# Kernel optimization log

Hardware: AMD Instinct MI355X
Metric: run time of the kernel (lower is better)

The kernel has to match this reference:

```python
import jax, jax.numpy as jnp
import numpy as np

BETA1 = 0.9
BETA2 = 0.8
THRESH = 1.0  # snntorch Leaky default threshold

T, B, NI, NH, NO = 100, 1024, 256, 512, 10


def setup_inputs() -> dict:
    key = jax.random.key(0)
    kx, k1, k2 = jax.random.split(key, 3)
    x = jax.random.normal(kx, (T, B, NI), dtype=jnp.float32)
    # Weight_synapse 'bin_random_prob' init: binary {0, w} with given probs
    W1 = (jax.random.uniform(k1, (NH, NI)) < 0.8).astype(jnp.float32) * 0.5
    W2 = (jax.random.uniform(k2, (NO, NH)) < 0.5).astype(jnp.float32) * 0.5
    return {"x": x, "W1": W1, "W2": W2}


def _lif(mem, cur, beta):
    # snntorch Leaky, reset_mechanism='subtract': reset from previous mem,
    # then mem = beta*mem + cur - reset*threshold; spk = heaviside(mem - thr)
    reset = (mem > THRESH).astype(cur.dtype)
    mem = beta * mem + cur - reset * THRESH
    spk = (mem > THRESH).astype(cur.dtype)
    return spk, mem


def reference(x, W1, W2):
    b = x.shape[1]
    mem1_0 = jnp.zeros((b, W1.shape[0]), x.dtype)
    mem2_0 = jnp.zeros((b, W2.shape[0]), x.dtype)

    def step(carry, xt):
        mem1, mem2 = carry
        cur1 = xt @ W1.T                      # [B, NH]
        spk1, mem1 = _lif(mem1, cur1, BETA1)
        cur2 = spk1 @ W2.T                    # [B, NO]
        spk2, mem2 = _lif(mem2, cur2, BETA2)
        return (mem1, mem2), (cur1, cur2, spk1, spk2, mem1, mem2)

    _, (cur1, cur2, spk1, spk2, mem1, mem2) = jax.lax.scan(step, (mem1_0, mem2_0), x)
    # matches {'cur':[c1,c2],'spks':[s1,s2],'mem':[m1,m2]}, each stacked on time
    return cur1, cur2, spk1, spk2, mem1, mem2
```

## Files before the change

kernel.cpp:

```cpp
#include <hip/hip_runtime.h>

#define TT 100
#define BB 1024
#define NI 256
#define NH 512
#define NO 10
#define TB (TT*BB)
#define GK 512
#define GN 512

constexpr long long C1_OFF = 0;
constexpr long long C2_OFF = 52428800LL;
constexpr long long S1_OFF = 53452800LL;
constexpr long long S2_OFF = 105881600LL;
constexpr long long M1_OFF = 106905600LL;
constexpr long long M2_OFF = 159334400LL;

typedef short bf16x8 __attribute__((ext_vector_type(8)));
typedef float f32x4 __attribute__((ext_vector_type(4)));

__device__ __forceinline__ unsigned int rne_bf16(float f) {
    unsigned int u = __float_as_uint(f);
    return (u + 0x7fffu + ((u >> 16) & 1u)) >> 16;
}

__device__ __forceinline__ unsigned int pack_hilo(float f) {
    unsigned int hi = rne_bf16(f);
    float hif = __uint_as_float(hi << 16);
    float e = f - hif;
    unsigned int lo = rne_bf16(e);
    return (hi & 0xffffu) | (lo << 16);
}

__device__ __forceinline__ void pack4(uint4& d, const float4& a) {
    d.x = pack_hilo(a.x); d.y = pack_hilo(a.y); d.z = pack_hilo(a.z); d.w = pack_hilo(a.w);
}

__device__ __forceinline__ void gload16(const void* g, void* l) {
    __builtin_amdgcn_global_load_lds(
        (const __attribute__((address_space(1))) void*)g,
        (__attribute__((address_space(3))) void*)l, 16, 0, 0);
}

__global__ void prep_w_kernel(const float* __restrict__ W1, short* __restrict__ Wimg) {
    int i = blockIdx.x * blockDim.x + threadIdx.x;
    if (i >= 4 * 16 * 128 * 4) return;
    int c16 = i & 3;
    int r   = (i >> 2) & 127;
    int kt  = (i >> 9) & 15;
    int p   = i >> 13;
    int usrc = c16 ^ ((r >> 1) & 3);
    int kbase = kt * 16 + usrc * 4;
    float4 w = *(const float4*)&W1[(long long)(p * 128 + r) * NI + kbase];
    float f[4] = {w.x, w.y, w.z, w.w};
    uint4 o;
    unsigned int* op = &o.x;
    #pragma unroll
    for (int j = 0; j < 4; ++j) {
        unsigned int hb = __float_as_uint(f[j]) >> 16;
        op[j] = hb | (hb << 16);
    }
    ((uint4*)Wimg)[i] = o;
}

__launch_bounds__(256, 2)
__global__ void gemm1_kernel(const float* __restrict__ x, const short* __restrict__ Wimg,
                             float* __restrict__ C) {
    __shared__ short As[2][128][40];
    __shared__ short Ws[2][128][32];
    const int tid = threadIdx.x;
    const int bid = blockIdx.x;
    const int x8 = bid & 7;
    const int g  = bid >> 3;
    const int p  = g & 3;
    const int panel = (g >> 2) * 8 + x8;
    const int m0 = (799 - panel) * 128;
    const int n0 = p * 128;
    const int wid = tid >> 6;
    const int lane = tid & 63;
    const int wm = (wid >> 1) * 64;
    const int wn = (wid & 1) * 64;

    f32x4 acc[4][4] = {};

    const int srow = tid >> 2;
    const int sc4 = tid & 3;
    const long long ax0 = (long long)(m0 + srow) * NI + sc4 * 4;
    const long long ax1 = ax0 + 64LL * NI;

    const int fr = lane & 15;
    const int fk = (lane >> 4) * 8;
    const int swz = (((lane >> 4) ^ ((fr >> 1) & 3)) << 4);

    const short* wbase = Wimg + (long long)p * 16 * 4096;
    const int c0 = wid * 2;

    gload16(wbase + (c0    ) * 512 + lane * 8, (char*)&Ws[0][0][0] + (c0    ) * 1024);
    gload16(wbase + (c0 + 1) * 512 + lane * 8, (char*)&Ws[0][0][0] + (c0 + 1) * 1024);
    uint4 pa0, pa1;
    {
        float4 t0a = *(const float4*)&x[ax0];
        float4 t0b = *(const float4*)&x[ax1];
        uint4 q0, q1;
        pack4(q0, t0a); pack4(q1, t0b);
        *(uint4*)&As[0][srow][sc4 * 8]      = q0;
        *(uint4*)&As[0][srow + 64][sc4 * 8] = q1;
        float4 t1a = *(const float4*)&x[ax0 + 16];
        float4 t1b = *(const float4*)&x[ax1 + 16];
        pack4(pa0, t1a); pack4(pa1, t1b);
    }
    float4 raw0a = *(const float4*)&x[ax0 + 32];
    float4 raw0b = *(const float4*)&x[ax1 + 32];
    float4 raw1a = *(const float4*)&x[ax0 + 48];
    float4 raw1b = *(const float4*)&x[ax1 + 48];
    __syncthreads();

    #pragma unroll
    for (int kt = 0; kt < 16; ++kt) {
        const int cur = kt & 1;
        const int nxt = cur ^ 1;

        if (kt + 1 < 16) {
            const short* wt = wbase + (kt + 1) * 4096;
            gload16(wt + (c0    ) * 512 + lane * 8, (char*)&Ws[nxt][0][0] + (c0    ) * 1024);
            gload16(wt + (c0 + 1) * 512 + lane * 8, (char*)&Ws[nxt][0][0] + (c0 + 1) * 1024);
            *(uint4*)&As[nxt][srow][sc4 * 8]      = pa0;
            *(uint4*)&As[nxt][srow + 64][sc4 * 8] = pa1;
        }
        if (kt + 2 < 16) {
            if (cur == 0) { pack4(pa0, raw0a); pack4(pa1, raw0b); }
            else          { pack4(pa0, raw1a); pack4(pa1, raw1b); }
        }
        if (kt + 4 < 16) {
            if (cur == 0) {
                raw0a = *(const float4*)&x[ax0 + (long long)(kt + 4) * 16];
                raw0b = *(const float4*)&x[ax1 + (long long)(kt + 4) * 16];
            } else {
                raw1a = *(const float4*)&x[ax0 + (long long)(kt + 4) * 16];
                raw1b = *(const float4*)&x[ax1 + (long long)(kt + 4) * 16];
            }
        }

        bf16x8 af[4], wf[4];
        #pragma unroll
        for (int i = 0; i < 4; ++i) {
            af[i] = *(const bf16x8*)&As[cur][wm + i * 16 + fr][fk];
            wf[i] = *(const bf16x8*)((const char*)&Ws[cur][wn + i * 16 + fr][0] + swz);
        }
        #pragma unroll
        for (int i = 0; i < 4; ++i)
            #pragma unroll
            for (int j = 0; j < 4; ++j)
                acc[i][j] = __builtin_amdgcn_mfma_f32_16x16x32_bf16(af[i], wf[j], acc[i][j], 0, 0, 0);

        if (kt + 1 < 16) __syncthreads();
    }

    const int col = lane & 15;
    const int rbase = (lane >> 4) * 4;
    #pragma unroll
    for (int i = 0; i < 4; ++i) {
        #pragma unroll
        for (int j = 0; j < 4; ++j) {
            long long base = (long long)(m0 + wm + i * 16 + rbase) * GN + (n0 + wn + j * 16 + col);
            #pragma unroll
            for (int r = 0; r < 4; ++r)
                C[base + (long long)r * GN] = acc[i][j][r];
        }
    }
}

__launch_bounds__(512)
__global__ void lif_kernel(const float* __restrict__ cur1, const float* __restrict__ W2,
                           float* __restrict__ out) {
    const int b = blockIdx.x;
    const int h = threadIdx.x;
    const int w = h >> 6;
    const int lane = h & 63;

    __shared__ unsigned long long wmks[2][8];
    __shared__ unsigned long long w2ms[NO][8];

    #pragma unroll
    for (int o = 0; o < NO; ++o) {
        unsigned long long mk = __ballot(W2[o * NH + h] != 0.0f);
        if (lane == 0) w2ms[o][w] = mk;
    }
    __syncthreads();
    unsigned long long w2m[8];
    if (h < NO) {
        #pragma unroll
        for (int i = 0; i < 8; ++i) w2m[i] = w2ms[h][i];
    }

    float m1 = 0.0f, m2 = 0.0f;
    const long long idx1 = (long long)b * NH + h;
    const float* c1p = cur1 + idx1;
    float* s1p = out + S1_OFF + idx1;
    float* m1p = out + M1_OFF + idx1;
    const long long st1 = (long long)BB * NH;

    float c1 = c1p[0];
    for (int t = 0; t < TT; ++t) {
        float c1n = 0.0f;
        if (t + 1 < TT) c1n = c1p[(long long)(t + 1) * st1];

        float rst = (m1 > 1.0f) ? 1.0f : 0.0f;
        m1 = 0.9f * m1 + c1 - rst;
        float s1 = (m1 > 1.0f) ? 1.0f : 0.0f;
        s1p[(long long)t * st1] = s1;
        m1p[(long long)t * st1] = m1;

        unsigned long long mk = __ballot(s1 != 0.0f);
        if (lane == 0) wmks[t & 1][w] = mk;
        __syncthreads();

        if (h < NO) {
            int cnt = 0;
            #pragma unroll
            for (int i = 0; i < 8; ++i) cnt += __popcll(wmks[t & 1][i] & w2m[i]);
            float c2 = 0.5f * (float)cnt;
            float rst2 = (m2 > 1.0f) ? 1.0f : 0.0f;
            m2 = 0.8f * m2 + c2 - rst2;
            float s2 = (m2 > 1.0f) ? 1.0f : 0.0f;
            long long o2 = (long long)t * (BB * NO) + b * NO + h;
            out[C2_OFF + o2] = c2;
            out[S2_OFF + o2] = s2;
            out[M2_OFF + o2] = m2;
        }
        c1 = c1n;
    }
}

extern "C" void kernel_launch(void* const* d_in, const int* in_sizes, int n_in,
                              void* d_out, int out_size, void* d_ws, size_t ws_size,
                              hipStream_t stream) {
    const float* x  = (const float*)d_in[0];
    const float* W1 = (const float*)d_in[1];
    const float* W2 = (const float*)d_in[2];
    float* out = (float*)d_out;

    short* Wp = (short*)(out + S1_OFF);
    float* C1 = out + C1_OFF;

    {
        int units = NH * GK / 8;
        prep_w_kernel<<<(units + 255) / 256, 256, 0, stream>>>(W1, Wp);
    }
    gemm1_kernel<<<(TB / 128) * (GN / 128), 256, 0, stream>>>(x, Wp, C1);
    lif_kernel<<<BB, NH, 0, stream>>>(C1, W2, out);
}
```

Measured before the change: 263.3 us.

## Overlap GEMM and LIF scan by chunking time into fused joint launches

Splits the time axis into four chunks and launches a joint kernel whose blocks are either GEMM tiles for chunk i or LIF recurrence blocks for chunk i-1. The LIF work then runs alongside the next chunk's GEMM instead of after the whole GEMM. The LIF role is rewritten to use 256 threads with two hidden units per thread, and it carries membrane state across chunks by reading back the previous chunk's stored mem outputs. The W1 image moves into the last chunk's spike region, which is only overwritten by the final launch. This adds extra launches and mixes two block roles with different resource profiles in one grid.

```diff
diff --git a/kernel.cpp b/kernel.cpp
--- a/kernel.cpp
+++ b/kernel.cpp
@@ -8,6 +8,8 @@
 #define TB (TT*BB)
 #define GK 512
 #define GN 512
+#define NCH 4
+#define TCH 25
 
 constexpr long long C1_OFF = 0;
 constexpr long long C2_OFF = 52428800LL;
@@ -63,18 +65,15 @@
     ((uint4*)Wimg)[i] = o;
 }
 
-__launch_bounds__(256, 2)
-__global__ void gemm1_kernel(const float* __restrict__ x, const short* __restrict__ Wimg,
-                             float* __restrict__ C) {
-    __shared__ short As[2][128][40];
-    __shared__ short Ws[2][128][32];
+__device__ __forceinline__ void gemm_role(
+    const float* __restrict__ xc, const short* __restrict__ Wimg, float* __restrict__ Cc,
+    int gid, int nPanels,
+    short (&As)[2][128][40], short (&Ws)[2][128][32])
+{
     const int tid = threadIdx.x;
-    const int bid = blockIdx.x;
-    const int x8 = bid & 7;
-    const int g  = bid >> 3;
-    const int p  = g & 3;
-    const int panel = (g >> 2) * 8 + x8;
-    const int m0 = (799 - panel) * 128;
+    const int p = gid & 3;
+    const int panel = gid >> 2;
+    const int m0 = (nPanels - 1 - panel) * 128;
     const int n0 = p * 128;
     const int wid = tid >> 6;
     const int lane = tid & 63;
@@ -99,20 +98,20 @@
     gload16(wbase + (c0 + 1) * 512 + lane * 8, (char*)&Ws[0][0][0] + (c0 + 1) * 1024);
     uint4 pa0, pa1;
     {
-        float4 t0a = *(const float4*)&x[ax0];
-        float4 t0b = *(const float4*)&x[ax1];
+        float4 t0a = *(const float4*)&xc[ax0];
+        float4 t0b = *(const float4*)&xc[ax1];
         uint4 q0, q1;
         pack4(q0, t0a); pack4(q1, t0b);
         *(uint4*)&As[0][srow][sc4 * 8]      = q0;
         *(uint4*)&As[0][srow + 64][sc4 * 8] = q1;
-        float4 t1a = *(const float4*)&x[ax0 + 16];
-        float4 t1b = *(const float4*)&x[ax1 + 16];
+        float4 t1a = *(const float4*)&xc[ax0 + 16];
+        float4 t1b = *(const float4*)&xc[ax1 + 16];
         pack4(pa0, t1a); pack4(pa1, t1b);
     }
-    float4 raw0a = *(const float4*)&x[ax0 + 32];
-    float4 raw0b = *(const float4*)&x[ax1 + 32];
-    float4 raw1a = *(const float4*)&x[ax0 + 48];
-    float4 raw1b = *(const float4*)&x[ax1 + 48];
+    float4 raw0a = *(const float4*)&xc[ax0 + 32];
+    float4 raw0b = *(const float4*)&xc[ax1 + 32];
+    float4 raw1a = *(const float4*)&xc[ax0 + 48];
+    float4 raw1b = *(const float4*)&xc[ax1 + 48];
     __syncthreads();
 
     #pragma unroll
@@ -133,11 +132,11 @@
         }
         if (kt + 4 < 16) {
             if (cur == 0) {
-                raw0a = *(const float4*)&x[ax0 + (long long)(kt + 4) * 16];
-                raw0b = *(const float4*)&x[ax1 + (long long)(kt + 4) * 16];
+                raw0a = *(const float4*)&xc[ax0 + (long long)(kt + 4) * 16];
+                raw0b = *(const float4*)&xc[ax1 + (long long)(kt + 4) * 16];
             } else {
-                raw1a = *(const float4*)&x[ax0 + (long long)(kt + 4) * 16];
-                raw1b = *(const float4*)&x[ax1 + (long long)(kt + 4) * 16];
+                raw1a = *(const float4*)&xc[ax0 + (long long)(kt + 4) * 16];
+                raw1b = *(const float4*)&xc[ax1 + (long long)(kt + 4) * 16];
             }
         }
 
@@ -165,57 +164,73 @@
             long long base = (long long)(m0 + wm + i * 16 + rbase) * GN + (n0 + wn + j * 16 + col);
             #pragma unroll
             for (int r = 0; r < 4; ++r)
-                C[base + (long long)r * GN] = acc[i][j][r];
-        }
-    }
-}
-
-__launch_bounds__(512)
-__global__ void lif_kernel(const float* __restrict__ cur1, const float* __restrict__ W2,
-                           float* __restrict__ out) {
-    const int b = blockIdx.x;
-    const int h = threadIdx.x;
-    const int w = h >> 6;
-    const int lane = h & 63;
-
-    __shared__ unsigned long long wmks[2][8];
-    __shared__ unsigned long long w2ms[NO][8];
+                Cc[base + (long long)r * GN] = acc[i][j][r];
+        }
+    }
+}
+
+__device__ __forceinline__ void lif_role(
+    const float* __restrict__ cur1, const float* __restrict__ W2, float* __restrict__ out,
+    int b, int t0, int t1,
+    unsigned long long (&wmks)[2][8], unsigned long long (&w2ms)[NO][8])
+{
+    const int tid = threadIdx.x;
+    const int w = tid >> 6;
+    const int lane = tid & 63;
+    const int h0 = tid, h1 = tid + 256;
 
     #pragma unroll
     for (int o = 0; o < NO; ++o) {
-        unsigned long long mk = __ballot(W2[o * NH + h] != 0.0f);
-        if (lane == 0) w2ms[o][w] = mk;
+        unsigned long long mk0 = __ballot(W2[o * NH + h0] != 0.0f);
+        unsigned long long mk1 = __ballot(W2[o * NH + h1] != 0.0f);
+        if (lane == 0) { w2ms[o][w] = mk0; w2ms[o][4 + w] = mk1; }
     }
     __syncthreads();
     unsigned long long w2m[8];
-    if (h < NO) {
+    if (tid < NO) {
         #pragma unroll
-        for (int i = 0; i < 8; ++i) w2m[i] = w2ms[h][i];
-    }
-
-    float m1 = 0.0f, m2 = 0.0f;
-    const long long idx1 = (long long)b * NH + h;
-    const float* c1p = cur1 + idx1;
-    float* s1p = out + S1_OFF + idx1;
-    float* m1p = out + M1_OFF + idx1;
+        for (int i = 0; i < 8; ++i) w2m[i] = w2ms[tid][i];
+    }
+
     const long long st1 = (long long)BB * NH;
-
-    float c1 = c1p[0];
-    for (int t = 0; t < TT; ++t) {
-        float c1n = 0.0f;
-        if (t + 1 < TT) c1n = c1p[(long long)(t + 1) * st1];
-
-        float rst = (m1 > 1.0f) ? 1.0f : 0.0f;
-        m1 = 0.9f * m1 + c1 - rst;
-        float s1 = (m1 > 1.0f) ? 1.0f : 0.0f;
-        s1p[(long long)t * st1] = s1;
-        m1p[(long long)t * st1] = m1;
-
-        unsigned long long mk = __ballot(s1 != 0.0f);
-        if (lane == 0) wmks[t & 1][w] = mk;
+    const long long i0 = (long long)b * NH + h0;
+    const long long i1 = (long long)b * NH + h1;
+    const float* cap = cur1 + i0;
+    const float* cbp = cur1 + i1;
+    float* sap = out + S1_OFF + i0;  float* sbp = out + S1_OFF + i1;
+    float* map = out + M1_OFF + i0;  float* mbp = out + M1_OFF + i1;
+
+    float m1a = 0.0f, m1b = 0.0f, m2 = 0.0f;
+    if (t0 != 0) {
+        m1a = map[(long long)(t0 - 1) * st1];
+        m1b = mbp[(long long)(t0 - 1) * st1];
+        if (tid < NO) m2 = out[M2_OFF + (long long)(t0 - 1) * (BB * NO) + b * NO + tid];
+    }
+
+    float ca = cap[(long long)t0 * st1];
+    float cb = cbp[(long long)t0 * st1];
+    for (int t = t0; t < t1; ++t) {
+        float can = 0.0f, cbn = 0.0f;
+        if (t + 1 < t1) {
+            can = cap[(long long)(t + 1) * st1];
+            cbn = cbp[(long long)(t + 1) * st1];
+        }
+
+        float rsta = (m1a > 1.0f) ? 1.0f : 0.0f;
+        m1a = 0.9f * m1a + ca - rsta;
+        float s1a = (m1a > 1.0f) ? 1.0f : 0.0f;
+        float rstb = (m1b > 1.0f) ? 1.0f : 0.0f;
+        m1b = 0.9f * m1b + cb - rstb;
+        float s1b = (m1b > 1.0f) ? 1.0f : 0.0f;
+        sap[(long long)t * st1] = s1a;  map[(long long)t * st1] = m1a;
+        sbp[(long long)t * st1] = s1b;  mbp[(long long)t * st1] = m1b;
+
+        unsigned long long mk0 = __ballot(s1a != 0.0f);
+        unsigned long long mk1 = __ballot(s1b != 0.0f);
+        if (lane == 0) { wmks[t & 1][w] = mk0; wmks[t & 1][4 + w] = mk1; }
         __syncthreads();
 
-        if (h < NO) {
+        if (tid < NO) {
             int cnt = 0;
             #pragma unroll
             for (int i = 0; i < 8; ++i) cnt += __popcll(wmks[t & 1][i] & w2m[i]);
@@ -223,12 +238,35 @@
             float rst2 = (m2 > 1.0f) ? 1.0f : 0.0f;
             m2 = 0.8f * m2 + c2 - rst2;
             float s2 = (m2 > 1.0f) ? 1.0f : 0.0f;
-            long long o2 = (long long)t * (BB * NO) + b * NO + h;
+            long long o2 = (long long)t * (BB * NO) + b * NO + tid;
             out[C2_OFF + o2] = c2;
             out[S2_OFF + o2] = s2;
             out[M2_OFF + o2] = m2;
         }
-        c1 = c1n;
+        ca = can; cb = cbn;
+    }
+}
+
+__launch_bounds__(256, 2)
+__global__ void joint_kernel(const float* __restrict__ xc, const short* __restrict__ Wimg,
+                             float* __restrict__ Cc, const float* __restrict__ cur1,
+                             const float* __restrict__ W2, float* __restrict__ out,
+                             int nPanels, int lifT0, int lifT1)
+{
+    __shared__ short As[2][128][40];
+    __shared__ short Ws[2][128][32];
+    __shared__ unsigned long long wmks[2][8];
+    __shared__ unsigned long long w2ms[NO][8];
+
+    const int bid = blockIdx.x;
+    const int G = nPanels * 4;
+    const int total = gridDim.x;
+    const long long a = (long long)bid * G / total;
+    const long long bc = (long long)(bid + 1) * G / total;
+    if (bc > a) {
+        gemm_role(xc, Wimg, Cc, (int)a, nPanels, As, Ws);
+    } else {
+        lif_role(cur1, W2, out, (int)(bid - bc), lifT0, lifT1, wmks, w2ms);
     }
 }
 
@@ -240,13 +278,23 @@
     const float* W2 = (const float*)d_in[2];
     float* out = (float*)d_out;
 
-    short* Wp = (short*)(out + S1_OFF);
+    short* Wp = (short*)(out + S1_OFF + (long long)(NCH - 1) * TCH * BB * NH);
     float* C1 = out + C1_OFF;
 
     {
         int units = NH * GK / 8;
         prep_w_kernel<<<(units + 255) / 256, 256, 0, stream>>>(W1, Wp);
     }
-    gemm1_kernel<<<(TB / 128) * (GN / 128), 256, 0, stream>>>(x, Wp, C1);
-    lif_kernel<<<BB, NH, 0, stream>>>(C1, W2, out);
-}
+    for (int i = 0; i <= NCH; ++i) {
+        const bool g = (i < NCH);
+        const bool l = (i >= 1);
+        const int gt0 = g ? i * TCH : 0;
+        const int nP  = g ? TCH * BB / 128 : 0;
+        const int G   = nP * 4;
+        const int L   = l ? BB : 0;
+        joint_kernel<<<G + L, 256, 0, stream>>>(
+            x + (long long)gt0 * BB * NI, Wp, C1 + (long long)gt0 * BB * GN,
+            C1, W2, out,
+            nP, l ? (i - 1) * TCH : 0, l ? i * TCH : 0);
+    }
+}
```

After: 382.2 us. 45.1% more time.

## Restructure LIF kernel to one wavefront per batch row with shuffle reductions

Applied to the files above, without the earlier changes.

The LIF scan kernel now maps each batch row to a single 64-lane wavefront, with each lane owning 8 hidden neurons. Layer-2 currents come from popcounts packed two per word and reduced with xor-shuffles, which removes the per-timestep block-wide __syncthreads and shared-memory ballot exchange. Loads and stores become float4-vectorized, and cur1 is prefetched two timesteps ahead. The cost is more registers per lane and a serial shuffle reduction chain at each step.

```diff
diff --git a/kernel.cpp b/kernel.cpp
--- a/kernel.cpp
+++ b/kernel.cpp
@@ -170,65 +170,101 @@
     }
 }
 
-__launch_bounds__(512)
+__launch_bounds__(256)
 __global__ void lif_kernel(const float* __restrict__ cur1, const float* __restrict__ W2,
                            float* __restrict__ out) {
-    const int b = blockIdx.x;
-    const int h = threadIdx.x;
-    const int w = h >> 6;
-    const int lane = h & 63;
-
-    __shared__ unsigned long long wmks[2][8];
-    __shared__ unsigned long long w2ms[NO][8];
-
+    const int tid = threadIdx.x;
+    const int lane = tid & 63;
+    const int b = blockIdx.x * 4 + (tid >> 6);
+
+    unsigned int w2b[NO];
     #pragma unroll
     for (int o = 0; o < NO; ++o) {
-        unsigned long long mk = __ballot(W2[o * NH + h] != 0.0f);
-        if (lane == 0) w2ms[o][w] = mk;
-    }
-    __syncthreads();
-    unsigned long long w2m[8];
-    if (h < NO) {
-        #pragma unroll
-        for (int i = 0; i < 8; ++i) w2m[i] = w2ms[h][i];
-    }
-
-    float m1 = 0.0f, m2 = 0.0f;
-    const long long idx1 = (long long)b * NH + h;
-    const float* c1p = cur1 + idx1;
-    float* s1p = out + S1_OFF + idx1;
-    float* m1p = out + M1_OFF + idx1;
+        unsigned int m = 0;
+        #pragma unroll
+        for (int j = 0; j < 8; ++j)
+            m |= (W2[o * NH + lane * 8 + j] != 0.0f) ? (1u << j) : 0u;
+        w2b[o] = m;
+    }
+
     const long long st1 = (long long)BB * NH;
-
-    float c1 = c1p[0];
-    for (int t = 0; t < TT; ++t) {
-        float c1n = 0.0f;
-        if (t + 1 < TT) c1n = c1p[(long long)(t + 1) * st1];
-
-        float rst = (m1 > 1.0f) ? 1.0f : 0.0f;
-        m1 = 0.9f * m1 + c1 - rst;
-        float s1 = (m1 > 1.0f) ? 1.0f : 0.0f;
-        s1p[(long long)t * st1] = s1;
-        m1p[(long long)t * st1] = m1;
-
-        unsigned long long mk = __ballot(s1 != 0.0f);
-        if (lane == 0) wmks[t & 1][w] = mk;
-        __syncthreads();
-
-        if (h < NO) {
-            int cnt = 0;
+    const long long idx = (long long)b * NH + lane * 8;
+    const float* c1p = cur1 + idx;
+    float* s1p = out + S1_OFF + idx;
+    float* m1p = out + M1_OFF + idx;
+
+    float m1[8] = {0.f, 0.f, 0.f, 0.f, 0.f, 0.f, 0.f, 0.f};
+    float m2[NO];
+    #pragma unroll
+    for (int o = 0; o < NO; ++o) m2[o] = 0.f;
+
+    float4 a0 = *(const float4*)&c1p[0];
+    float4 a1 = *(const float4*)&c1p[4];
+    float4 b0 = *(const float4*)&c1p[st1];
+    float4 b1 = *(const float4*)&c1p[st1 + 4];
+
+    auto stepT = [&](int t, const float4& x0, const float4& x1) {
+        const float cv[8] = {x0.x, x0.y, x0.z, x0.w, x1.x, x1.y, x1.z, x1.w};
+        float s1v[8];
+        unsigned int bits = 0;
+        #pragma unroll
+        for (int j = 0; j < 8; ++j) {
+            float rst = (m1[j] > 1.0f) ? 1.0f : 0.0f;
+            m1[j] = 0.9f * m1[j] + cv[j] - rst;
+            float s = (m1[j] > 1.0f) ? 1.0f : 0.0f;
+            s1v[j] = s;
+            bits |= (s != 0.0f) ? (1u << j) : 0u;
+        }
+        float4 sq0 = {s1v[0], s1v[1], s1v[2], s1v[3]};
+        float4 sq1 = {s1v[4], s1v[5], s1v[6], s1v[7]};
+        float4 mq0 = {m1[0], m1[1], m1[2], m1[3]};
+        float4 mq1 = {m1[4], m1[5], m1[6], m1[7]};
+        *(float4*)&s1p[(long long)t * st1]     = sq0;
+        *(float4*)&s1p[(long long)t * st1 + 4] = sq1;
+        *(float4*)&m1p[(long long)t * st1]     = mq0;
+        *(float4*)&m1p[(long long)t * st1 + 4] = mq1;
+
+        unsigned int pk[5];
+        #pragma unroll
+        for (int q = 0; q < 5; ++q)
+            pk[q] = (unsigned int)__popc(bits & w2b[2 * q])
+                  | ((unsigned int)__popc(bits & w2b[2 * q + 1]) << 16);
+        #pragma unroll
+        for (int s = 1; s < 64; s <<= 1) {
             #pragma unroll
-            for (int i = 0; i < 8; ++i) cnt += __popcll(wmks[t & 1][i] & w2m[i]);
+            for (int q = 0; q < 5; ++q)
+                pk[q] += __shfl_xor(pk[q], s);
+        }
+
+        float myc2 = 0.f, mys2 = 0.f, mym2 = 0.f;
+        #pragma unroll
+        for (int o = 0; o < NO; ++o) {
+            unsigned int cnt = (o & 1) ? (pk[o >> 1] >> 16) : (pk[o >> 1] & 0xffffu);
             float c2 = 0.5f * (float)cnt;
-            float rst2 = (m2 > 1.0f) ? 1.0f : 0.0f;
-            m2 = 0.8f * m2 + c2 - rst2;
-            float s2 = (m2 > 1.0f) ? 1.0f : 0.0f;
-            long long o2 = (long long)t * (BB * NO) + b * NO + h;
-            out[C2_OFF + o2] = c2;
-            out[S2_OFF + o2] = s2;
-            out[M2_OFF + o2] = m2;
-        }
-        c1 = c1n;
+            float rst2 = (m2[o] > 1.0f) ? 1.0f : 0.0f;
+            m2[o] = 0.8f * m2[o] + c2 - rst2;
+            float s2 = (m2[o] > 1.0f) ? 1.0f : 0.0f;
+            if (lane == o) { myc2 = c2; mys2 = s2; mym2 = m2[o]; }
+        }
+        if (lane < NO) {
+            long long o2 = (long long)t * (BB * NO) + (long long)b * NO + lane;
+            out[C2_OFF + o2] = myc2;
+            out[S2_OFF + o2] = mys2;
+            out[M2_OFF + o2] = mym2;
+        }
+    };
+
+    for (int t = 0; t < TT; t += 2) {
+        float4 na0 = {}, na1 = {}, nb0 = {}, nb1 = {};
+        if (t + 2 < TT) {
+            na0 = *(const float4*)&c1p[(long long)(t + 2) * st1];
+            na1 = *(const float4*)&c1p[(long long)(t + 2) * st1 + 4];
+            nb0 = *(const float4*)&c1p[(long long)(t + 3) * st1];
+            nb1 = *(const float4*)&c1p[(long long)(t + 3) * st1 + 4];
+        }
+        stepT(t,     a0, a1);
+        stepT(t + 1, b0, b1);
+        a0 = na0; a1 = na1; b0 = nb0; b1 = nb1;
     }
 }
 
@@ -248,5 +284,5 @@
         prep_w_kernel<<<(units + 255) / 256, 256, 0, stream>>>(W1, Wp);
     }
     gemm1_kernel<<<(TB / 128) * (GN / 128), 256, 0, stream>>>(x, Wp, C1);
-    lif_kernel<<<BB, NH, 0, stream>>>(C1, W2, out);
-}
+    lif_kernel<<<BB / 4, 256, 0, stream>>>(C1, W2, out);
+}
```

Measured after the change: 263.2 us. Within noise of the previous version (-0.0%).
